# Optimization experiments

Hardware: AMD Instinct MI355X
Metric: run time of the kernel (lower is better)

The kernel has to match this reference:

```python
import jax, jax.numpy as jnp
import numpy as np

EPS = 1e-5

def _conv(x, w, pad):
    return jax.lax.conv_general_dilated(
        x, w, window_strides=(1, 1), padding=((pad, pad), (pad, pad)),
        dimension_numbers=('NCHW', 'OIHW', 'NCHW'))

def _dyn_branch(x, w, d):
    # x: [N,C,H,W]; w: [N,9,H,W] softmax weights; d: dilation.
    # Equivalent to unfold(k=3, dilation=d, padding=d) + bmm with w,
    # done as 9 shifted zero-padded slices (row-major kernel order).
    N, C, H, W = x.shape
    xp = jnp.pad(x, ((0, 0), (0, 0), (d, d), (d, d)))
    out = jnp.zeros_like(x)
    k = 0
    for dy in (-d, 0, d):
        for dx in (-d, 0, d):
            patch = xp[:, :, d + dy:d + dy + H, d + dx:d + dx + W]
            out = out + patch * w[:, k:k + 1]
            k += 1
    return out

def setup_inputs() -> dict:
    key = jax.random.key(0)
    k1, k2, k3 = jax.random.split(key, 3)
    C = 256
    x = jax.random.normal(k1, (2, C, 96, 96), dtype=jnp.float32)
    W_cat = jax.random.normal(k2, (45, C, 3, 3), dtype=jnp.float32) * 0.05
    W_scale = jax.random.normal(k3, (C, 6 * C, 1, 1), dtype=jnp.float32) * 0.05
    gamma = jnp.ones((C,), dtype=jnp.float32)
    beta = jnp.zeros((C,), dtype=jnp.float32)
    return {"x": x, "W_cat": W_cat, "W_scale": W_scale, "gamma": gamma, "beta": beta}

def reference(x, W_cat, W_scale, gamma, beta):
    guidance = _conv(x, W_cat, pad=1)  # [N,45,H,W]
    outs = [x]
    for i, d in enumerate((1, 6, 12, 24, 36)):
        w = jax.nn.softmax(guidance[:, 9 * i:9 * (i + 1)], axis=1)  # [N,9,H,W]
        outs.append(_dyn_branch(x, w, d))
    cat = jnp.concatenate(outs, axis=1)  # [N, 6C, H, W]
    y = _conv(cat, W_scale, pad=0)       # [N, C, H, W]
    # BatchNorm2d in training mode (batch statistics, biased variance)
    mean = jnp.mean(y, axis=(0, 2, 3), keepdims=True)
    var = jnp.var(y, axis=(0, 2, 3), keepdims=True)
    y = (y - mean) * jax.lax.rsqrt(var + EPS)
    return y * gamma[None, :, None, None] + beta[None, :, None, None]
```

## Files before the change

### kernel.cpp

```cpp
#include <hip/hip_runtime.h>

typedef __bf16 bf16x8 __attribute__((ext_vector_type(8)));
typedef float f32x4 __attribute__((ext_vector_type(4)));

#define HW 9216
#define ZSLAB 9216
#define XTILE 32768

__device__ __forceinline__ unsigned short f2bf(float f) {
  unsigned u = __float_as_uint(f);
  unsigned r = (u + 0x7FFFu + ((u >> 16) & 1u)) >> 16;
  return (unsigned short)r;
}
__device__ __forceinline__ float bf2f(unsigned short h) {
  return __uint_as_float(((unsigned)h) << 16);
}

__device__ __forceinline__ void async16(const unsigned short* g, unsigned short* l) {
  __builtin_amdgcn_global_load_lds(
      (const __attribute__((address_space(1))) unsigned int*)g,
      (__attribute__((address_space(3))) unsigned int*)l, 16, 0, 0);
}

template <int O>
__device__ __forceinline__ void tapfma(float* y, uint4 lo, uint4 hi, uint4 wv) {
  const unsigned short* lu = (const unsigned short*)&lo;
  const unsigned short* hu = (const unsigned short*)&hi;
  const unsigned short* wu = (const unsigned short*)&wv;
#pragma unroll
  for (int j = 0; j < 8; ++j) {
    unsigned short zz = (O + j < 8) ? lu[O + j] : hu[O + j - 8];
    y[j] += bf2f(wu[j]) * bf2f(zz);
  }
}

template <int B, int D>
__device__ __forceinline__ void branch9(float* y, const unsigned short* zslab,
                                        const unsigned short* gb, int h, int w0) {
#define TAPK(K, DY, DX)                                                       \
  {                                                                           \
    int hh = h + (DY);                                                        \
    int hc = min(max(hh, 0), 95);                                             \
    const unsigned short* zr = zslab + hc * 96;                               \
    constexpr int O = (40 + (DX)) & 7;                                        \
    int s_col = w0 + (DX)-O;                               \
    int scl = min(max(s_col, 0), 88);                                         \
    int sch = min(max(s_col + 8, 0), 88);                                     \
    uint4 lo = *(const uint4*)(zr + scl);                                     \
    uint4 hi = *(const uint4*)(zr + sch);                                     \
    uint4 wv = *(const uint4*)(gb + (size_t)(((B - 1) * 9 + (K)) * 2) * HW);  \
    if ((unsigned)hh >= 96u) wv = make_uint4(0u, 0u, 0u, 0u);                 \
    if ((unsigned)s_col > 88u) lo = make_uint4(0u, 0u, 0u, 0u);               \
    if ((unsigned)(s_col + 8) > 88u) hi = make_uint4(0u, 0u, 0u, 0u);         \
    tapfma<O>(y, lo, hi, wv);                                                 \
  }
  TAPK(0, -D, -D) TAPK(1, -D, 0) TAPK(2, -D, D)
  TAPK(3, 0, -D)  TAPK(4, 0, 0)  TAPK(5, 0, D)
  TAPK(6, D, -D)  TAPK(7, D, 0)  TAPK(8, D, D)
#undef TAPK
}

__global__ __launch_bounds__(256) void init_all(const float* __restrict__ x,
                                                const float* __restrict__ Ws,
                                                const float* __restrict__ Wc,
                                                unsigned short* __restrict__ xb,
                                                unsigned short* __restrict__ Wsb,
                                                unsigned short* __restrict__ Wcb) {
  __shared__ float tile[64][65];
  int id = blockIdx.x;
  int t = threadIdx.x;
  if (id < 1152) {
    int bx = id % 144, by = (id / 144) % 4, n = id / 576;
    int p0 = bx * 64, ci0 = by * 64;
    int cl = t & 63, q = t >> 6;
#pragma unroll
    for (int i = 0; i < 16; ++i) {
      int cir = q + i * 4;
      tile[cir][cl] = x[((size_t)(n * 256 + ci0 + cir)) * HW + p0 + cl];
    }
    __syncthreads();
    int R = n * HW + p0 + cl;
    int Rt = R >> 7, Rl = R & 127;
#pragma unroll
    for (int i = 0; i < 2; ++i) {
      int cloc = q * 2 + i;
      unsigned rr[4];
#pragma unroll
      for (int jj = 0; jj < 4; ++jj) {
        unsigned short a = f2bf(tile[cloc * 8 + jj * 2][cl]);
        unsigned short b = f2bf(tile[cloc * 8 + jj * 2 + 1][cl]);
        rr[jj] = (unsigned)a | ((unsigned)b << 16);
      }
      *(uint4*)(xb + (size_t)Rt * XTILE + (by * 8 + cloc) * 1024 + Rl * 8) =
          make_uint4(rr[0], rr[1], rr[2], rr[3]);
    }
  } else {
    int u = (id - 1152) * 256 + t;
    if (u < 393216) {
      int r = u >> 8, k = u & 255;
      Wsb[(size_t)(r >> 7) * XTILE + (k >> 3) * 1024 + (r & 127) * 8 + (k & 7)] =
          f2bf(Ws[(size_t)(r & 255) * 1536 + (r >> 8) * 256 + k]);
    } else {
      int v = u - 393216;
      if (v < 110592) {
        int co = v / 2304, rr = v % 2304;
        int j = rr >> 8, ci = rr & 255;
        Wcb[v] = (co < 45) ? f2bf(Wc[(size_t)co * 2304 + ci * 9 + j]) : (unsigned short)0;
      }
    }
  }
}

__global__ __launch_bounds__(256) void gemms(const unsigned short* __restrict__ xb,
                                             const unsigned short* __restrict__ Wsb,
                                             const unsigned short* __restrict__ Wcb,
                                             unsigned short* __restrict__ z,
                                             unsigned short* __restrict__ gsmb) {
  __shared__ unsigned short smem[16384];
  int id = blockIdx.x;
  int t = threadIdx.x;
  int wid = t >> 6, lane = t & 63;
  int q = lane >> 4, ln = lane & 15;

  if (id < 288) {
    unsigned short* As = smem;
    unsigned short* Bs = smem + 4096;
    int m0 = id * 64;
    int mm = t >> 2, kq = t & 3;
    int m = m0 + mm;
    int img = m / HW, p = m % HW;
    int h = p / 96, w = p % 96;
    int mbase = img * HW;
    int nn = t >> 2;
    f32x4 acc[3] = {};
    uint4 aA0, aA1, aB0, aB1;

    {
      int hh = h - 1, ww = w - 1;
      bool valid = ((unsigned)hh < 96u) & ((unsigned)ww < 96u);
      int R = mbase + hh * 96 + ww;
      const unsigned short* pa =
          xb + (long)(R >> 7) * XTILE + kq * 1024 + (R & 127) * 8;
      aA0 = valid ? *(const uint4*)pa : make_uint4(0, 0, 0, 0);
      aA1 = valid ? *(const uint4*)(pa + 4096) : make_uint4(0, 0, 0, 0);
      if (t < 192) {
        const unsigned short* pb = Wcb + (size_t)nn * 2304 + kq * 8;
        aB0 = *(const uint4*)pb;
        aB1 = *(const uint4*)(pb + 32);
      }
    }

    for (int s = 0; s < 36; ++s) {
      ((uint4*)As)[kq * 64 + mm] = aA0;
      ((uint4*)As)[(kq + 4) * 64 + mm] = aA1;
      if (t < 192) {
        ((uint4*)Bs)[kq * 48 + nn] = aB0;
        ((uint4*)Bs)[(kq + 4) * 48 + nn] = aB1;
      }
      __syncthreads();
      if (s + 1 < 36) {
        int s1 = s + 1;
        int j = s1 >> 2;
        int hh = h + j / 3 - 1, ww = w + j % 3 - 1;
        bool valid = ((unsigned)hh < 96u) & ((unsigned)ww < 96u);
        int R = mbase + hh * 96 + ww;
        const unsigned short* pa = xb + (long)(R >> 7) * XTILE +
                                   ((s1 & 3) * 8 + kq) * 1024 + (R & 127) * 8;
        aA0 = valid ? *(const uint4*)pa : make_uint4(0, 0, 0, 0);
        aA1 = valid ? *(const uint4*)(pa + 4096) : make_uint4(0, 0, 0, 0);
        if (t < 192) {
          const unsigned short* pb = Wcb + (size_t)nn * 2304 + s1 * 64 + kq * 8;
          aB0 = *(const uint4*)pb;
          aB1 = *(const uint4*)(pb + 32);
        }
      }
#pragma unroll
      for (int kk = 0; kk < 2; ++kk) {
        bf16x8 a = ((const bf16x8*)As)[(kk * 4 + q) * 64 + wid * 16 + ln];
#pragma unroll
        for (int fn = 0; fn < 3; ++fn) {
          bf16x8 b = ((const bf16x8*)Bs)[(kk * 4 + q) * 48 + fn * 16 + ln];
          acc[fn] = __builtin_amdgcn_mfma_f32_16x16x32_bf16(a, b, acc[fn], 0, 0, 0);
        }
      }
      __syncthreads();
    }

    float* LDSf = (float*)smem;
#pragma unroll
    for (int fn = 0; fn < 3; ++fn)
#pragma unroll
      for (int r = 0; r < 4; ++r)
        LDSf[(wid * 16 + q * 4 + r) * 49 + fn * 16 + ln] = acc[fn][r];
    __syncthreads();
    if (t < 64) {
      const float* row = LDSf + t * 49;
      int mg = m0 + t;
      int img2 = mg / HW, p2 = mg - img2 * HW;
      for (int grp = 0; grp < 5; ++grp) {
        float v[9], mx = -1e30f;
#pragma unroll
        for (int k = 0; k < 9; ++k) { v[k] = row[grp * 9 + k]; mx = fmaxf(mx, v[k]); }
        float sum = 0.f;
#pragma unroll
        for (int k = 0; k < 9; ++k) { v[k] = __expf(v[k] - mx); sum += v[k]; }
        float inv = 1.f / sum;
#pragma unroll
        for (int k = 0; k < 9; ++k) {
          int col = grp * 9 + k;
          gsmb[((size_t)(col * 2 + img2)) * HW + p2] = f2bf(v[k] * inv);
        }
      }
    }
  } else {
    int zid = id - 288;
    int mt = zid % 144, ct = zid / 144;
    int m0 = mt * 128, c0 = ct * 128;
    int wm = (wid >> 1) * 64, wn = (wid & 1) * 64;
    bool isB = wid >= 2;
    const unsigned short* gsrc =
        (isB ? Wsb + (size_t)ct * XTILE : xb + (size_t)mt * XTILE) + lane * 8;
    unsigned short* lb = smem + (isB ? 8192 : 0);
    int ow = (wid & 1) * 4;
    f32x4 acc[4][4] = {};

#pragma unroll
    for (int kq = 0; kq < 4; ++kq)
      async16(gsrc + (ow + kq) * 512, lb + (ow + kq) * 512);
    __syncthreads();

    for (int s = 0; s < 8; ++s) {
      int cur = s & 1, nxt = cur ^ 1;
      if (s < 7) {
#pragma unroll
        for (int kq = 0; kq < 4; ++kq)
          async16(gsrc + (s + 1) * 4096 + (ow + kq) * 512,
                  lb + nxt * 4096 + (ow + kq) * 512);
      }
      const unsigned short* Asc = smem + cur * 4096;
      const unsigned short* Bsc = smem + 8192 + cur * 4096;
      bf16x8 a[4], b[4];
#pragma unroll
      for (int f = 0; f < 4; ++f) {
        a[f] = ((const bf16x8*)Asc)[q * 128 + wm + f * 16 + ln];
        b[f] = ((const bf16x8*)Bsc)[q * 128 + wn + f * 16 + ln];
      }
#pragma unroll
      for (int fm = 0; fm < 4; ++fm)
#pragma unroll
        for (int fn = 0; fn < 4; ++fn)
          acc[fm][fn] = __builtin_amdgcn_mfma_f32_16x16x32_bf16(a[fm], b[fn], acc[fm][fn], 0, 0, 0);
      __syncthreads();
    }

    int sl = c0 >> 8, cb = c0 & 255;
    int img = m0 / HW;
    int pbase = m0 - img * HW;
#pragma unroll
    for (int fm = 0; fm < 4; ++fm) {
      int p = pbase + wm + fm * 16 + q * 4;
#pragma unroll
      for (int fn = 0; fn < 4; ++fn) {
        int ch = cb + wn + fn * 16 + ln;
        size_t slab = ((size_t)(sl * 256 + ch) * 2 + img) * ZSLAB;
        unsigned lo = (unsigned)f2bf(acc[fm][fn][0]) | ((unsigned)f2bf(acc[fm][fn][1]) << 16);
        unsigned hi = (unsigned)f2bf(acc[fm][fn][2]) | ((unsigned)f2bf(acc[fm][fn][3]) << 16);
        *(uint2*)(z + slab + p) = make_uint2(lo, hi);
      }
    }
  }
}

__global__ __launch_bounds__(384) void accum_chw(const unsigned short* __restrict__ z,
                                                 const unsigned short* __restrict__ gsmb,
                                                 float* __restrict__ yacc,
                                                 float* __restrict__ stats) {
  __shared__ float red[12];
  int t = threadIdx.x;
  int wq = t % 12, hl = t / 12;
  int h = blockIdx.x * 32 + hl;
  int img = blockIdx.y, ch = blockIdx.z;
  int w0 = wq * 8;
  int p0 = h * 96 + w0;
  const unsigned short* gb = gsmb + (size_t)img * HW + p0;

  float y[8] = {0.f, 0.f, 0.f, 0.f, 0.f, 0.f, 0.f, 0.f};
  {
    const unsigned short* zs = z + ((size_t)(ch * 2 + img)) * ZSLAB;
    uint4 v = *(const uint4*)(zs + p0);
    const unsigned short* u = (const unsigned short*)&v;
#pragma unroll
    for (int j = 0; j < 8; ++j) y[j] += bf2f(u[j]);
  }
  size_t chslab = (size_t)(ch * 2 + img) * ZSLAB;
  branch9<1, 1>(y, z + (size_t)(1 * 512) * ZSLAB + chslab, gb, h, w0);
  branch9<2, 6>(y, z + (size_t)(2 * 512) * ZSLAB + chslab, gb, h, w0);
  branch9<3, 12>(y, z + (size_t)(3 * 512) * ZSLAB + chslab, gb, h, w0);
  branch9<4, 24>(y, z + (size_t)(4 * 512) * ZSLAB + chslab, gb, h, w0);
  branch9<5, 36>(y, z + (size_t)(5 * 512) * ZSLAB + chslab, gb, h, w0);

  size_t ybase = ((size_t)(img * 256 + ch)) * HW + p0;
  *(float4*)(yacc + ybase) = make_float4(y[0], y[1], y[2], y[3]);
  *(float4*)(yacc + ybase + 4) = make_float4(y[4], y[5], y[6], y[7]);

  float s1 = 0.f, s2 = 0.f;
#pragma unroll
  for (int j = 0; j < 8; ++j) { s1 += y[j]; s2 += y[j] * y[j]; }
#pragma unroll
  for (int off = 1; off <= 32; off <<= 1) {
    s1 += __shfl_xor(s1, off);
    s2 += __shfl_xor(s2, off);
  }
  int wid = t >> 6, lane = t & 63;
  if (lane == 0) { red[wid] = s1; red[6 + wid] = s2; }
  __syncthreads();
  if (t == 0) {
    float a = red[0] + red[1] + red[2] + red[3] + red[4] + red[5];
    atomicAdd(&stats[ch], a);
  } else if (t == 64) {
    float b = red[6] + red[7] + red[8] + red[9] + red[10] + red[11];
    atomicAdd(&stats[256 + ch], b);
  }
}

__global__ __launch_bounds__(256) void bn_apply(const float* __restrict__ yacc,
                                                const float* __restrict__ stats,
                                                const float* __restrict__ gamma,
                                                const float* __restrict__ beta,
                                                float* __restrict__ out) {
  int q = blockIdx.x * 256 + threadIdx.x;
  int ch = (q / 2304) & 255;
  const float inv_cnt = 1.f / 18432.f;
  float mean = stats[ch] * inv_cnt;
  float var = stats[256 + ch] * inv_cnt - mean * mean;
  float sc = rsqrtf(var + 1e-5f) * gamma[ch];
  float sh = beta[ch] - mean * sc;
  float4 v = *(const float4*)(yacc + (size_t)q * 4);
  float4 o = make_float4(v.x * sc + sh, v.y * sc + sh, v.z * sc + sh, v.w * sc + sh);
  *(float4*)(out + (size_t)q * 4) = o;
}

extern "C" void kernel_launch(void* const* d_in, const int* in_sizes, int n_in,
                              void* d_out, int out_size, void* d_ws, size_t ws_size,
                              hipStream_t stream) {
  const float* x = (const float*)d_in[0];
  const float* Wc = (const float*)d_in[1];
  const float* Ws = (const float*)d_in[2];
  const float* gamma = (const float*)d_in[3];
  const float* beta = (const float*)d_in[4];
  float* out = (float*)d_out;

  unsigned short* xb = (unsigned short*)d_ws;
  unsigned short* Wsb = xb + 4718592;
  unsigned short* Wcb = Wsb + 393216;
  unsigned short* gsmb = Wcb + 110592;
  unsigned short* z = gsmb + 829440;
  float* yacc = (float*)(z + 28311552);
  float* stats = yacc + 4718592;

  hipMemsetAsync(stats, 0, 512 * sizeof(float), stream);
  init_all<<<3120, 256, 0, stream>>>(x, Ws, Wc, xb, Wsb, Wcb);
  gemms<<<2016, 256, 0, stream>>>(xb, Wsb, Wcb, z, gsmb);
  accum_chw<<<dim3(3, 2, 256), 384, 0, stream>>>(z, gsmb, yacc, stats);
  bn_apply<<<4608, 256, 0, stream>>>(yacc, stats, gamma, beta, out);
}
```

Baseline: 172.0 us.

## Share row loads across taps and remap accum_chw threads to 16 pixels

The dynamic-dilation accumulation kernel now loads each needed 8-wide bf16 chunk of a row once and reuses it for all three horizontal taps, instead of issuing two loads per tap. Out-of-bounds loads are redirected to a zeroed guard slot past the stats buffer rather than loading then masking. Threads are remapped to a flat 1D grid of 128-thread blocks, each covering 16 pixels in two halves. The shared-memory reduction and barrier are replaced by per-wavefront atomics. This trades fewer memory instructions and no block barrier for more atomics on the stats and a larger per-thread working set.

```diff
diff --git a/kernel.cpp b/kernel.cpp
--- a/kernel.cpp
+++ b/kernel.cpp
@@ -35,29 +35,62 @@
 }
 
 template <int B, int D>
-__device__ __forceinline__ void branch9(float* y, const unsigned short* zslab,
-                                        const unsigned short* gb, int h, int w0) {
-#define TAPK(K, DY, DX)                                                       \
-  {                                                                           \
-    int hh = h + (DY);                                                        \
-    int hc = min(max(hh, 0), 95);                                             \
-    const unsigned short* zr = zslab + hc * 96;                               \
-    constexpr int O = (40 + (DX)) & 7;                                        \
-    int s_col = w0 + (DX)-O;                               \
-    int scl = min(max(s_col, 0), 88);                                         \
-    int sch = min(max(s_col + 8, 0), 88);                                     \
-    uint4 lo = *(const uint4*)(zr + scl);                                     \
-    uint4 hi = *(const uint4*)(zr + sch);                                     \
-    uint4 wv = *(const uint4*)(gb + (size_t)(((B - 1) * 9 + (K)) * 2) * HW);  \
-    if ((unsigned)hh >= 96u) wv = make_uint4(0u, 0u, 0u, 0u);                 \
-    if ((unsigned)s_col > 88u) lo = make_uint4(0u, 0u, 0u, 0u);               \
-    if ((unsigned)(s_col + 8) > 88u) hi = make_uint4(0u, 0u, 0u, 0u);         \
-    tapfma<O>(y, lo, hi, wv);                                                 \
-  }
-  TAPK(0, -D, -D) TAPK(1, -D, 0) TAPK(2, -D, D)
-  TAPK(3, 0, -D)  TAPK(4, 0, 0)  TAPK(5, 0, D)
-  TAPK(6, D, -D)  TAPK(7, D, 0)  TAPK(8, D, D)
-#undef TAPK
+__device__ __forceinline__ void branch8(float* y, const unsigned short* __restrict__ z,
+                                        unsigned slab, unsigned guard,
+                                        const unsigned short* __restrict__ gb,
+                                        int h, int w0) {
+  constexpr int NW = (D == 12 || D == 36) ? 5 : 3;
+  int cc[NW];
+  if constexpr (D == 1 || D == 6) {
+    cc[0] = w0 - 8; cc[1] = w0; cc[2] = w0 + 8;
+  } else if constexpr (D == 12) {
+    cc[0] = w0 - 16; cc[1] = w0 - 8; cc[2] = w0; cc[3] = w0 + 8; cc[4] = w0 + 16;
+  } else if constexpr (D == 24) {
+    cc[0] = w0 - 24; cc[1] = w0; cc[2] = w0 + 24;
+  } else {
+    cc[0] = w0 - 40; cc[1] = w0 - 32; cc[2] = w0; cc[3] = w0 + 32; cc[4] = w0 + 40;
+  }
+  bool cv[NW];
+#pragma unroll
+  for (int k = 0; k < NW; ++k) cv[k] = ((unsigned)cc[k] <= 88u);
+
+#pragma unroll
+  for (int r = 0; r < 3; ++r) {
+    int hh = h + (r - 1) * D;
+    bool rv = ((unsigned)hh < 96u);
+    unsigned rbase = slab + (unsigned)(hh * 96);
+    uint4 W[NW];
+#pragma unroll
+    for (int k = 0; k < NW; ++k) {
+      unsigned idx = (rv && cv[k]) ? (rbase + (unsigned)cc[k]) : guard;
+      W[k] = *(const uint4*)(z + idx);
+    }
+    const int K0 = (B - 1) * 9 + r * 3;
+    uint4 wv0 = *(const uint4*)(gb + (size_t)((K0 + 0) * 2) * HW);
+    uint4 wv1 = *(const uint4*)(gb + (size_t)((K0 + 1) * 2) * HW);
+    uint4 wv2 = *(const uint4*)(gb + (size_t)((K0 + 2) * 2) * HW);
+    if constexpr (D == 1) {
+      tapfma<7>(y, W[0], W[1], wv0);
+      tapfma<0>(y, W[1], W[1], wv1);
+      tapfma<1>(y, W[1], W[2], wv2);
+    } else if constexpr (D == 6) {
+      tapfma<2>(y, W[0], W[1], wv0);
+      tapfma<0>(y, W[1], W[1], wv1);
+      tapfma<6>(y, W[1], W[2], wv2);
+    } else if constexpr (D == 12) {
+      tapfma<4>(y, W[0], W[1], wv0);
+      tapfma<0>(y, W[2], W[2], wv1);
+      tapfma<4>(y, W[3], W[4], wv2);
+    } else if constexpr (D == 24) {
+      tapfma<0>(y, W[0], W[0], wv0);
+      tapfma<0>(y, W[1], W[1], wv1);
+      tapfma<0>(y, W[2], W[2], wv2);
+    } else {
+      tapfma<4>(y, W[0], W[1], wv0);
+      tapfma<0>(y, W[2], W[2], wv1);
+      tapfma<4>(y, W[3], W[4], wv2);
+    }
+  }
 }
 
 __global__ __launch_bounds__(256) void init_all(const float* __restrict__ x,
@@ -271,55 +304,60 @@
   }
 }
 
-__global__ __launch_bounds__(384) void accum_chw(const unsigned short* __restrict__ z,
-                                                 const unsigned short* __restrict__ gsmb,
-                                                 float* __restrict__ yacc,
-                                                 float* __restrict__ stats) {
-  __shared__ float red[12];
-  int t = threadIdx.x;
-  int wq = t % 12, hl = t / 12;
-  int h = blockIdx.x * 32 + hl;
-  int img = blockIdx.y, ch = blockIdx.z;
-  int w0 = wq * 8;
-  int p0 = h * 96 + w0;
-  const unsigned short* gb = gsmb + (size_t)img * HW + p0;
-
-  float y[8] = {0.f, 0.f, 0.f, 0.f, 0.f, 0.f, 0.f, 0.f};
-  {
-    const unsigned short* zs = z + ((size_t)(ch * 2 + img)) * ZSLAB;
-    uint4 v = *(const uint4*)(zs + p0);
-    const unsigned short* u = (const unsigned short*)&v;
-#pragma unroll
-    for (int j = 0; j < 8; ++j) y[j] += bf2f(u[j]);
-  }
-  size_t chslab = (size_t)(ch * 2 + img) * ZSLAB;
-  branch9<1, 1>(y, z + (size_t)(1 * 512) * ZSLAB + chslab, gb, h, w0);
-  branch9<2, 6>(y, z + (size_t)(2 * 512) * ZSLAB + chslab, gb, h, w0);
-  branch9<3, 12>(y, z + (size_t)(3 * 512) * ZSLAB + chslab, gb, h, w0);
-  branch9<4, 24>(y, z + (size_t)(4 * 512) * ZSLAB + chslab, gb, h, w0);
-  branch9<5, 36>(y, z + (size_t)(5 * 512) * ZSLAB + chslab, gb, h, w0);
+__global__ __launch_bounds__(128, 5) void accum_chw(const unsigned short* __restrict__ z,
+                                                    const unsigned short* __restrict__ gsmb,
+                                                    float* __restrict__ yacc,
+                                                    float* __restrict__ stats,
+                                                    unsigned guard) {
+  int cid = blockIdx.x * 128 + threadIdx.x;
+  int img = cid >= 147456;
+  int rem = cid - img * 147456;
+  int ch = rem / 576;
+  int pc = rem - ch * 576;
+  int h = pc / 6;
+  int w16 = (pc - h * 6) * 16;
+  int p0 = h * 96 + w16;
+
+  unsigned chsl = (unsigned)(ch * 2 + img) * ZSLAB;
+  const unsigned short* gb0 = gsmb + (size_t)img * HW + p0;
+
+  float y[16];
+#pragma unroll 1
+  for (int hf = 0; hf < 2; ++hf) {
+    float* yh = y + hf * 8;
+    int w0 = w16 + hf * 8;
+    unsigned ph = (unsigned)(p0 + hf * 8);
+    const unsigned short* gb = gb0 + hf * 8;
+    {
+      uint4 v = *(const uint4*)(z + chsl + ph);
+      const unsigned short* u = (const unsigned short*)&v;
+#pragma unroll
+      for (int j = 0; j < 8; ++j) yh[j] = bf2f(u[j]);
+    }
+    branch8<1, 1>(yh, z, chsl + 512u * ZSLAB, guard, gb, h, w0);
+    branch8<2, 6>(yh, z, chsl + 1024u * ZSLAB, guard, gb, h, w0);
+    branch8<3, 12>(yh, z, chsl + 1536u * ZSLAB, guard, gb, h, w0);
+    branch8<4, 24>(yh, z, chsl + 2048u * ZSLAB, guard, gb, h, w0);
+    branch8<5, 36>(yh, z, chsl + 2560u * ZSLAB, guard, gb, h, w0);
+  }
 
   size_t ybase = ((size_t)(img * 256 + ch)) * HW + p0;
   *(float4*)(yacc + ybase) = make_float4(y[0], y[1], y[2], y[3]);
   *(float4*)(yacc + ybase + 4) = make_float4(y[4], y[5], y[6], y[7]);
+  *(float4*)(yacc + ybase + 8) = make_float4(y[8], y[9], y[10], y[11]);
+  *(float4*)(yacc + ybase + 12) = make_float4(y[12], y[13], y[14], y[15]);
 
   float s1 = 0.f, s2 = 0.f;
 #pragma unroll
-  for (int j = 0; j < 8; ++j) { s1 += y[j]; s2 += y[j] * y[j]; }
+  for (int j = 0; j < 16; ++j) { s1 += y[j]; s2 += y[j] * y[j]; }
 #pragma unroll
   for (int off = 1; off <= 32; off <<= 1) {
     s1 += __shfl_xor(s1, off);
     s2 += __shfl_xor(s2, off);
   }
-  int wid = t >> 6, lane = t & 63;
-  if (lane == 0) { red[wid] = s1; red[6 + wid] = s2; }
-  __syncthreads();
-  if (t == 0) {
-    float a = red[0] + red[1] + red[2] + red[3] + red[4] + red[5];
-    atomicAdd(&stats[ch], a);
-  } else if (t == 64) {
-    float b = red[6] + red[7] + red[8] + red[9] + red[10] + red[11];
-    atomicAdd(&stats[256 + ch], b);
+  if ((threadIdx.x & 63) == 0) {
+    atomicAdd(&stats[ch], s1);
+    atomicAdd(&stats[256 + ch], s2);
   }
 }
 
@@ -357,10 +395,11 @@
   unsigned short* z = gsmb + 829440;
   float* yacc = (float*)(z + 28311552);
   float* stats = yacc + 4718592;
-
-  hipMemsetAsync(stats, 0, 512 * sizeof(float), stream);
+  const unsigned guard_idx = 28311552u + 9437184u + 1024u;
+
+  hipMemsetAsync(stats, 0, 512 * sizeof(float) + 256, stream);
   init_all<<<3120, 256, 0, stream>>>(x, Ws, Wc, xb, Wsb, Wcb);
   gemms<<<2016, 256, 0, stream>>>(xb, Wsb, Wcb, z, gsmb);
-  accum_chw<<<dim3(3, 2, 256), 384, 0, stream>>>(z, gsmb, yacc, stats);
+  accum_chw<<<2304, 128, 0, stream>>>(z, gsmb, yacc, stats, guard_idx);
   bn_apply<<<4608, 256, 0, stream>>>(yacc, stats, gamma, beta, out);
 }
```

Result: slower. 591.2 us (+243.8%).
